# Optimization experiments

Measured on AMD Instinct MI355X. Metric: run time of the kernel, lower is better.

The kernel has to match this reference:

```python
import jax, jax.numpy as jnp
import numpy as np

RADIUS = 0.4
SIGMA = 0.08
EPS = 1e-5  # InstanceNorm2d default eps
KERNEL_CONDENSE_RATIO = 0.7


def setup_inputs() -> dict:
    key = jax.random.key(0)
    k1, k2, k3, k4, k5 = jax.random.split(key, 5)
    m, b, nc, ks, na, co = 1024, 2, 512, 24, 60, 128
    frag = jax.random.uniform(k1, (m, 3), dtype=jnp.float32)          # fragment points in unit cube
    clouds = jax.random.uniform(k2, (b, 3, nc), dtype=jnp.float32)    # centers (already n_center -> no FPS)
    # kernel points inside ball of KERNEL_CONDENSE_RATIO * radius
    kp = (jax.random.uniform(k3, (ks, 3), dtype=jnp.float32) - 0.5) * 2.0 * (KERNEL_CONDENSE_RATIO * RADIUS)
    # kanchor=60 rotation anchors (random orthonormal frames via QR)
    anchors, _ = jnp.linalg.qr(jax.random.normal(k4, (na, 3, 3), dtype=jnp.float32))
    # rotate kernel points per anchor: (ks, na, 3), matching np.transpose(anchors @ kernels.T, (2,0,1))
    kernels = jnp.einsum('aij,kj->kai', anchors, kp)
    # BasicSO3Conv weight: dim_in=1 -> W [dim_out, ks]
    W = jax.random.normal(k5, (co, ks), dtype=jnp.float32) * (1.0 / np.sqrt(ks))
    return {"frag": frag, "clouds": clouds, "kernels": kernels, "W": W, "anchors": anchors}


def _propagate(frag, clouds, kernels, W):
    # frag [m,3], clouds [b,3,nc], kernels [ks,na,3], W [co,ks]
    c = jnp.transpose(clouds, (0, 2, 1))                 # [b,nc,3]
    diff = frag[None, None] - c[:, :, None]              # [b,nc,m,3] (frag point minus center)
    d2 = jnp.sum(diff * diff, axis=-1)                   # [b,nc,m]
    mask = (d2 < RADIUS * RADIUS).astype(diff.dtype)     # ball query mask
    nnctn = jnp.sum(mask, axis=-1)                       # [b,nc] neighbor counts
    base = jnp.exp(-d2 / SIGMA) * mask                   # shared Gaussian factor, masked [b,nc,m]
    k2 = jnp.sum(kernels * kernels, axis=-1)             # [ks,na]
    na = kernels.shape[1]

    def step(carry, a_idx):
        kpa = kernels[:, a_idx]                          # [ks,3] kernel points for this anchor
        dot = jnp.einsum('bnmd,kd->bnmk', diff, kpa)     # [b,nc,m,ks]
        # exp(-||diff - kp||^2 / sigma) = base * exp((2*dot - |kp|^2)/sigma)
        w = base[..., None] * jnp.exp((2.0 * dot - k2[:, a_idx]) / SIGMA)
        return carry, jnp.sum(w, axis=2)                 # [b,nc,ks]

    _, wts = jax.lax.scan(step, 0, jnp.arange(na))       # [na,b,nc,ks]
    wts = jnp.transpose(wts, (1, 3, 2, 0))               # [b,ks,nc,na]
    wts = wts / (nnctn[:, None, :, None] + 1.0)          # count normalization

    feats = jnp.einsum('ck,bkna->bcna', W, wts)          # BasicSO3Conv (dim_in=1): [b,co,nc,na]
    # InstanceNorm2d(affine=False): per (b, channel) stats over spatial (nc, na)
    mu = jnp.mean(feats, axis=(2, 3), keepdims=True)
    var = jnp.var(feats, axis=(2, 3), keepdims=True)
    feat = (feats - mu) * jax.lax.rsqrt(var + EPS)
    return jax.nn.relu(feat)


def reference(frag, clouds, kernels, W, anchors):
    feat = _propagate(frag, clouds, kernels, W)
    # SphericalPointCloud(xyz=centers, feats, anchors)
    return clouds, feat, anchors
```

## Files before the change

### kernel.cpp

```cpp
#include <hip/hip_runtime.h>
#include <math.h>

#define NC 512
#define NB 2
#define M 1024
#define KS 24
#define NA 60
#define CO 128
#define CELLS 1440
#define CCELLS 480
#define NTOT 30720.0f
#define LSCALE 18.033688011112043f
#define R2 0.16f
#define NSLOT 32

#define FEAT_OFF 3072
#define ANCH_OFF (3072 + 7864320)
#define FLP 61

typedef float __attribute__((ext_vector_type(2))) f32x2;

__device__ __forceinline__ float dot4acc(float s, float4 w, float4 v) {
    return fmaf(w.x, v.x, fmaf(w.y, v.y, fmaf(w.z, v.z, fmaf(w.w, v.w, s))));
}

#define PK_FMA(d, a, b, c) \
    asm("v_pk_fma_f32 %0, %1, %2, %3" : "=v"(d) : "v"(a), "v"(b), "v"(c))

__launch_bounds__(256)
__global__ void k_wts(const float* __restrict__ frag, const float* __restrict__ clouds,
                      const float* __restrict__ kernels, const float* __restrict__ W,
                      float* __restrict__ wts, float* __restrict__ accum) {
    int bx = blockIdx.x;
    int chunk = bx % 3;
    int bn = bx / 3;
    int b = bn >> 9, n = bn & (NC - 1);
    int tid = threadIdx.x, wave = tid >> 6, lane = tid & 63;
    __shared__ __align__(8) float sdxf[M + 2], sdyf[M + 2], sdzf[M + 2], seif[M + 2];
    __shared__ int wcnt[16];
    __shared__ __align__(16) float swl[512];

    int lc0 = tid, lc1 = tid + 256;
    float4 kc0, kc1;
    {
        int cells[2] = {chunk * CCELLS + lc0, chunk * CCELLS + lc1};
        bool vld[2] = {true, lc1 < CCELLS};
        float4* kcs[2] = {&kc0, &kc1};
        #pragma unroll
        for (int q = 0; q < 2; ++q) {
            if (vld[q]) {
                int cell = cells[q];
                int a = cell / KS, k = cell - a * KS;
                const float* kp = kernels + (size_t)(k * NA + a) * 3;
                float kx = kp[0], ky = kp[1], kz = kp[2];
                float k2 = kx * kx + ky * ky + kz * kz;
                *kcs[q] = make_float4(kx * (2.0f * LSCALE), ky * (2.0f * LSCALE),
                                      kz * (2.0f * LSCALE), -k2 * LSCALE);
            } else {
                *kcs[q] = make_float4(0.f, 0.f, 0.f, -1e30f);
            }
        }
    }

    float cx = clouds[b * 3 * NC + n];
    float cy = clouds[b * 3 * NC + NC + n];
    float cz = clouds[b * 3 * NC + 2 * NC + n];

    float dx[4], dy[4], dz[4], ev[4];
    int pos[4];
    bool pr[4];
    unsigned long long lmask = (1ull << lane) - 1ull;
    #pragma unroll
    for (int j = 0; j < 4; ++j) {
        int m = tid + j * 256;
        dx[j] = frag[3 * m]     - cx;
        dy[j] = frag[3 * m + 1] - cy;
        dz[j] = frag[3 * m + 2] - cz;
        float s = __fmul_rn(dx[j], dx[j]);
        s = __fadd_rn(s, __fmul_rn(dy[j], dy[j]));
        s = __fadd_rn(s, __fmul_rn(dz[j], dz[j]));
        pr[j] = s < R2;
        ev[j] = __builtin_amdgcn_exp2f(-s * LSCALE);
        unsigned long long mk = __ballot(pr[j]);
        pos[j] = __popcll(mk & lmask);
        if (lane == 0) wcnt[j * 4 + wave] = __popcll(mk);
    }
    __syncthreads();
    int run = 0, base[4];
    #pragma unroll
    for (int t2 = 0; t2 < 16; ++t2) {
        if ((t2 & 3) == wave) base[t2 >> 2] = run;
        run += wcnt[t2];
    }
    int cnt = run;
    #pragma unroll
    for (int j = 0; j < 4; ++j)
        if (pr[j]) {
            int p = base[j] + pos[j];
            sdxf[p] = dx[j]; sdyf[p] = dy[j]; sdzf[p] = dz[j]; seif[p] = ev[j];
        }
    if (tid == 0) {
        sdxf[cnt] = 0.f; sdyf[cnt] = 0.f; sdzf[cnt] = 0.f; seif[cnt] = 0.f;
    }
    __syncthreads();

    f32x2 Kx0 = {kc0.x, kc0.x}, Ky0 = {kc0.y, kc0.y}, Kz0 = {kc0.z, kc0.z}, Kw0 = {kc0.w, kc0.w};
    f32x2 Kx1 = {kc1.x, kc1.x}, Ky1 = {kc1.y, kc1.y}, Kz1 = {kc1.z, kc1.z}, Kw1 = {kc1.w, kc1.w};
    f32x2 a0p = {0.f, 0.f}, a1p = {0.f, 0.f};
    const f32x2* dx2 = (const f32x2*)sdxf;
    const f32x2* dy2 = (const f32x2*)sdyf;
    const f32x2* dz2 = (const f32x2*)sdzf;
    const f32x2* ei2 = (const f32x2*)seif;
    int np = (cnt + 1) >> 1;
    #pragma unroll 2
    for (int i = 0; i < np; ++i) {
        f32x2 Pdx = dx2[i], Pdy = dy2[i], Pdz = dz2[i], Pei = ei2[i];
        f32x2 t0, t1, e0, e1;
        PK_FMA(t0, Pdz, Kz0, Kw0);
        PK_FMA(t0, Pdy, Ky0, t0);
        PK_FMA(t0, Pdx, Kx0, t0);
        PK_FMA(t1, Pdz, Kz1, Kw1);
        PK_FMA(t1, Pdy, Ky1, t1);
        PK_FMA(t1, Pdx, Kx1, t1);
        e0.x = __builtin_amdgcn_exp2f(t0.x);
        e0.y = __builtin_amdgcn_exp2f(t0.y);
        e1.x = __builtin_amdgcn_exp2f(t1.x);
        e1.y = __builtin_amdgcn_exp2f(t1.y);
        PK_FMA(a0p, e0, Pei, a0p);
        PK_FMA(a1p, e1, Pei, a1p);
    }
    float acc0 = a0p.x + a0p.y;
    float acc1 = a1p.x + a1p.y;

    float inv = 1.0f / (float)(cnt + 1);
    float w0 = acc0 * inv, w1 = acc1 * inv;
    float* wrow = wts + (size_t)bn * CELLS + chunk * CCELLS;
    wrow[lc0] = w0;
    swl[lc0] = w0;
    if (lc1 < CCELLS) { wrow[lc1] = w1; swl[lc1] = w1; }
    __syncthreads();

    int c = tid >> 1, ah = tid & 1;
    float4 wr[6];
    {
        const float4* W4 = (const float4*)(W + c * KS);
        #pragma unroll
        for (int j = 0; j < 6; ++j) wr[j] = W4[j];
    }
    float fs = 0.f, fs2 = 0.f;
    #pragma unroll
    for (int i = 0; i < 10; ++i) {
        const float4* v4 = (const float4*)(swl + (ah * 10 + i) * KS);
        float f = 0.f;
        #pragma unroll
        for (int j = 0; j < 6; ++j) f = dot4acc(f, wr[j], v4[j]);
        fs += f;
        fs2 = fmaf(f, f, fs2);
    }
    fs  += __shfl_xor(fs, 1);
    fs2 += __shfl_xor(fs2, 1);
    if (ah == 0) {
        int slot = bx & (NSLOT - 1);
        float* ap = accum + (((size_t)(b * NSLOT + slot) * CO + c) * 2);
        atomicAdd(&ap[0], fs);
        atomicAdd(&ap[1], fs2);
    }
}

__launch_bounds__(256)
__global__ void k_out(const float* __restrict__ wts, const float* __restrict__ W,
                      const float* __restrict__ accum, const float* __restrict__ clouds,
                      const float* __restrict__ anchors, float* __restrict__ out) {
    int bid = blockIdx.x;
    int bn = bid >> 1, ch = bid & 1;
    int b = bn >> 9, n = bn & (NC - 1);
    int tid = threadIdx.x, wave = tid >> 6, lane = tid & 63;
    __shared__ __align__(16) float wl[CELLS];
    __shared__ float fl[64 * FLP];
    __shared__ float4 sred[256];
    __shared__ float2 sst[64];

    if (bid < 12) {
        int i = bid * 256 + tid;
        out[i] = clouds[i];
    } else if (bid < 15) {
        int i = (bid - 12) * 256 + tid;
        if (i < 540) out[ANCH_OFF + i] = anchors[i];
    }

    {
        const float4* src = (const float4*)(wts + (size_t)bn * CELLS);
        float4* wl4 = (float4*)wl;
        wl4[tid] = src[tid];
        if (tid < 104) wl4[tid + 256] = src[tid + 256];
    }

    {
        int cp = tid & 31, sg = tid >> 5;
        const float4* A4 = (const float4*)accum;
        float4 r = make_float4(0.f, 0.f, 0.f, 0.f);
        #pragma unroll
        for (int s = 0; s < 4; ++s) {
            float4 v = A4[((size_t)(b * NSLOT + sg * 4 + s)) * 64 + ch * 32 + cp];
            r.x += v.x; r.y += v.y; r.z += v.z; r.w += v.w;
        }
        sred[tid] = r;
    }
    __syncthreads();

    if (tid < 32) {
        float4 r = make_float4(0.f, 0.f, 0.f, 0.f);
        #pragma unroll
        for (int g = 0; g < 8; ++g) {
            float4 v = sred[tid + 32 * g];
            r.x += v.x; r.y += v.y; r.z += v.z; r.w += v.w;
        }
        const float pz = 32.0f * __uint_as_float(0xAAAAAAAAu);
        r.x -= pz; r.y -= pz; r.z -= pz; r.w -= pz;
        const float invN = 1.0f / NTOT;
        float mu0 = r.x * invN;
        float var0 = fmaxf(fmaf(-mu0, mu0, r.y * invN), 0.f);
        float mu1 = r.z * invN;
        float var1 = fmaxf(fmaf(-mu1, mu1, r.w * invN), 0.f);
        sst[2 * tid]     = make_float2(mu0, rsqrtf(var0 + 1e-5f));
        sst[2 * tid + 1] = make_float2(mu1, rsqrtf(var1 + 1e-5f));
    }

    int c_loc = tid >> 2, aq = tid & 3;
    int c = ch * 64 + c_loc;
    float4 wr[6];
    {
        const float4* W4 = (const float4*)(W + c * KS);
        #pragma unroll
        for (int j = 0; j < 6; ++j) wr[j] = W4[j];
    }
    __syncthreads();
    float2 st = sst[c_loc];

    #pragma unroll
    for (int i = 0; i < 15; ++i) {
        int a = aq * 15 + i;
        const float4* v4 = (const float4*)(wl + a * KS);
        float f = 0.f;
        #pragma unroll
        for (int j = 0; j < 6; ++j) f = dot4acc(f, wr[j], v4[j]);
        fl[c_loc * FLP + a] = fmaxf((f - st.x) * st.y, 0.f);
    }
    __syncthreads();

    #pragma unroll 4
    for (int i = 0; i < 16; ++i) {
        int cl = wave * 16 + i;
        if (lane < NA)
            out[FEAT_OFF + (((size_t)(b * CO + ch * 64 + cl)) * NC + n) * NA + lane]
                = fl[cl * FLP + lane];
    }
}

extern "C" void kernel_launch(void* const* d_in, const int* in_sizes, int n_in,
                              void* d_out, int out_size, void* d_ws, size_t ws_size,
                              hipStream_t stream) {
    const float* frag    = (const float*)d_in[0];
    const float* clouds  = (const float*)d_in[1];
    const float* kernels = (const float*)d_in[2];
    const float* W       = (const float*)d_in[3];
    const float* anchors = (const float*)d_in[4];
    float* out = (float*)d_out;

    char* ws = (char*)d_ws;
    float* wts   = (float*)(ws);
    float* accum = (float*)(ws + 5898240);

    k_wts<<<3 * NB * NC, 256, 0, stream>>>(frag, clouds, kernels, W, wts, accum);
    k_out<<<2 * NB * NC, 256, 0, stream>>>(wts, W, accum, clouds, anchors, out);
}
```

Measured before the change: 134.2 us.

## Split cells into two chunks with three cells per thread and interleaved LDS

The weight kernel now splits the 1440 kernel-anchor cells into two chunks of 768 instead of three of 480, so each thread evaluates three cells per neighbor point. This cuts the launch from 3 to 2 blocks per center. That reduces the repeated per-block work of computing frag distances and compacting neighbors, and reuses each point load across more cells. Neighbor data is stored interleaved as pairs in one LDS array so each point pair is fetched with two float4 loads. In exchange, more padded cells are wasted in the last chunk and each thread holds more registers.

```diff
diff --git a/kernel.cpp b/kernel.cpp
--- a/kernel.cpp
+++ b/kernel.cpp
@@ -8,7 +8,7 @@
 #define NA 60
 #define CO 128
 #define CELLS 1440
-#define CCELLS 480
+#define CCELLS 768
 #define NTOT 30720.0f
 #define LSCALE 18.033688011112043f
 #define R2 0.16f
@@ -32,33 +32,26 @@
                       const float* __restrict__ kernels, const float* __restrict__ W,
                       float* __restrict__ wts, float* __restrict__ accum) {
     int bx = blockIdx.x;
-    int chunk = bx % 3;
-    int bn = bx / 3;
+    int bn = bx >> 1, chunk = bx & 1;
     int b = bn >> 9, n = bn & (NC - 1);
     int tid = threadIdx.x, wave = tid >> 6, lane = tid & 63;
-    __shared__ __align__(8) float sdxf[M + 2], sdyf[M + 2], sdzf[M + 2], seif[M + 2];
+    __shared__ __align__(16) float spp[(M / 2 + 2) * 8];
     __shared__ int wcnt[16];
-    __shared__ __align__(16) float swl[512];
-
-    int lc0 = tid, lc1 = tid + 256;
-    float4 kc0, kc1;
-    {
-        int cells[2] = {chunk * CCELLS + lc0, chunk * CCELLS + lc1};
-        bool vld[2] = {true, lc1 < CCELLS};
-        float4* kcs[2] = {&kc0, &kc1};
-        #pragma unroll
-        for (int q = 0; q < 2; ++q) {
-            if (vld[q]) {
-                int cell = cells[q];
-                int a = cell / KS, k = cell - a * KS;
-                const float* kp = kernels + (size_t)(k * NA + a) * 3;
-                float kx = kp[0], ky = kp[1], kz = kp[2];
-                float k2 = kx * kx + ky * ky + kz * kz;
-                *kcs[q] = make_float4(kx * (2.0f * LSCALE), ky * (2.0f * LSCALE),
-                                      kz * (2.0f * LSCALE), -k2 * LSCALE);
-            } else {
-                *kcs[q] = make_float4(0.f, 0.f, 0.f, -1e30f);
-            }
+    __shared__ __align__(16) float swl[CCELLS];
+
+    float4 kc[3];
+    #pragma unroll
+    for (int q = 0; q < 3; ++q) {
+        int cell = chunk * CCELLS + tid + q * 256;
+        if (cell < CELLS) {
+            int a = cell / KS, k = cell - a * KS;
+            const float* kp = kernels + (size_t)(k * NA + a) * 3;
+            float kx = kp[0], ky = kp[1], kz = kp[2];
+            float k2 = kx * kx + ky * ky + kz * kz;
+            kc[q] = make_float4(kx * (2.0f * LSCALE), ky * (2.0f * LSCALE),
+                                kz * (2.0f * LSCALE), -k2 * LSCALE);
+        } else {
+            kc[q] = make_float4(0.f, 0.f, 0.f, -1e30f);
         }
     }
 
@@ -97,47 +90,59 @@
     for (int j = 0; j < 4; ++j)
         if (pr[j]) {
             int p = base[j] + pos[j];
-            sdxf[p] = dx[j]; sdyf[p] = dy[j]; sdzf[p] = dz[j]; seif[p] = ev[j];
+            float* sp = spp + (p >> 1) * 8 + (p & 1);
+            sp[0] = dx[j]; sp[2] = dy[j]; sp[4] = dz[j]; sp[6] = ev[j];
         }
     if (tid == 0) {
-        sdxf[cnt] = 0.f; sdyf[cnt] = 0.f; sdzf[cnt] = 0.f; seif[cnt] = 0.f;
-    }
-    __syncthreads();
-
-    f32x2 Kx0 = {kc0.x, kc0.x}, Ky0 = {kc0.y, kc0.y}, Kz0 = {kc0.z, kc0.z}, Kw0 = {kc0.w, kc0.w};
-    f32x2 Kx1 = {kc1.x, kc1.x}, Ky1 = {kc1.y, kc1.y}, Kz1 = {kc1.z, kc1.z}, Kw1 = {kc1.w, kc1.w};
-    f32x2 a0p = {0.f, 0.f}, a1p = {0.f, 0.f};
-    const f32x2* dx2 = (const f32x2*)sdxf;
-    const f32x2* dy2 = (const f32x2*)sdyf;
-    const f32x2* dz2 = (const f32x2*)sdzf;
-    const f32x2* ei2 = (const f32x2*)seif;
+        #pragma unroll
+        for (int pp = 0; pp < 2; ++pp) {
+            int p = cnt + pp;
+            float* sp = spp + (p >> 1) * 8 + (p & 1);
+            sp[0] = 0.f; sp[2] = 0.f; sp[4] = 0.f; sp[6] = 0.f;
+        }
+    }
+    __syncthreads();
+
+    f32x2 Kx[3], Ky[3], Kz[3], Kw[3], acc[3];
+    #pragma unroll
+    for (int q = 0; q < 3; ++q) {
+        Kx[q].x = kc[q].x; Kx[q].y = kc[q].x;
+        Ky[q].x = kc[q].y; Ky[q].y = kc[q].y;
+        Kz[q].x = kc[q].z; Kz[q].y = kc[q].z;
+        Kw[q].x = kc[q].w; Kw[q].y = kc[q].w;
+        acc[q].x = 0.f; acc[q].y = 0.f;
+    }
+    const float4* pp4 = (const float4*)spp;
     int np = (cnt + 1) >> 1;
     #pragma unroll 2
     for (int i = 0; i < np; ++i) {
-        f32x2 Pdx = dx2[i], Pdy = dy2[i], Pdz = dz2[i], Pei = ei2[i];
-        f32x2 t0, t1, e0, e1;
-        PK_FMA(t0, Pdz, Kz0, Kw0);
-        PK_FMA(t0, Pdy, Ky0, t0);
-        PK_FMA(t0, Pdx, Kx0, t0);
-        PK_FMA(t1, Pdz, Kz1, Kw1);
-        PK_FMA(t1, Pdy, Ky1, t1);
-        PK_FMA(t1, Pdx, Kx1, t1);
-        e0.x = __builtin_amdgcn_exp2f(t0.x);
-        e0.y = __builtin_amdgcn_exp2f(t0.y);
-        e1.x = __builtin_amdgcn_exp2f(t1.x);
-        e1.y = __builtin_amdgcn_exp2f(t1.y);
-        PK_FMA(a0p, e0, Pei, a0p);
-        PK_FMA(a1p, e1, Pei, a1p);
-    }
-    float acc0 = a0p.x + a0p.y;
-    float acc1 = a1p.x + a1p.y;
+        float4 q0 = pp4[2 * i];
+        float4 q1 = pp4[2 * i + 1];
+        f32x2 Pdx; Pdx.x = q0.x; Pdx.y = q0.y;
+        f32x2 Pdy; Pdy.x = q0.z; Pdy.y = q0.w;
+        f32x2 Pdz; Pdz.x = q1.x; Pdz.y = q1.y;
+        f32x2 Pei; Pei.x = q1.z; Pei.y = q1.w;
+        #pragma unroll
+        for (int q = 0; q < 3; ++q) {
+            f32x2 t, e;
+            PK_FMA(t, Pdz, Kz[q], Kw[q]);
+            PK_FMA(t, Pdy, Ky[q], t);
+            PK_FMA(t, Pdx, Kx[q], t);
+            e.x = __builtin_amdgcn_exp2f(t.x);
+            e.y = __builtin_amdgcn_exp2f(t.y);
+            PK_FMA(acc[q], e, Pei, acc[q]);
+        }
+    }
 
     float inv = 1.0f / (float)(cnt + 1);
-    float w0 = acc0 * inv, w1 = acc1 * inv;
     float* wrow = wts + (size_t)bn * CELLS + chunk * CCELLS;
-    wrow[lc0] = w0;
-    swl[lc0] = w0;
-    if (lc1 < CCELLS) { wrow[lc1] = w1; swl[lc1] = w1; }
+    #pragma unroll
+    for (int q = 0; q < 3; ++q) {
+        float w = (acc[q].x + acc[q].y) * inv;
+        int lc = tid + q * 256;
+        swl[lc] = w;
+        if (chunk * CCELLS + lc < CELLS) wrow[lc] = w;
+    }
     __syncthreads();
 
     int c = tid >> 1, ah = tid & 1;
@@ -149,8 +154,8 @@
     }
     float fs = 0.f, fs2 = 0.f;
     #pragma unroll
-    for (int i = 0; i < 10; ++i) {
-        const float4* v4 = (const float4*)(swl + (ah * 10 + i) * KS);
+    for (int i = 0; i < 16; ++i) {
+        const float4* v4 = (const float4*)(swl + (ah * 16 + i) * KS);
         float f = 0.f;
         #pragma unroll
         for (int j = 0; j < 6; ++j) f = dot4acc(f, wr[j], v4[j]);
@@ -271,6 +276,6 @@
     float* wts   = (float*)(ws);
     float* accum = (float*)(ws + 5898240);
 
-    k_wts<<<3 * NB * NC, 256, 0, stream>>>(frag, clouds, kernels, W, wts, accum);
+    k_wts<<<2 * NB * NC, 256, 0, stream>>>(frag, clouds, kernels, W, wts, accum);
     k_out<<<2 * NB * NC, 256, 0, stream>>>(wts, W, accum, clouds, anchors, out);
 }
```

Result: no change. 135.7 us (+1.1%).
